# Performance work log

Hardware: AMD Instinct MI355X
Metric: run time of the kernel (lower is better)

## Reference

```python
import jax, jax.numpy as jnp
import numpy as np

BATCH = 2048
IN_DIM = 512          # group input dim
HID = 1024            # meta_output_dim = dim*2
E = 16                # meta_experts_num = num_experts*2
RANK = 2              # lora_rank
EPS = 1e-5


def setup_inputs() -> dict:
    key = jax.random.key(0)
    ks = jax.random.split(key, 8)
    x = jax.random.normal(ks[0], (BATCH, IN_DIM), jnp.float32)
    gate_states = jax.random.normal(ks[1], (BATCH, IN_DIM), jnp.float32)
    expert_indices = jnp.arange(E, dtype=jnp.int64)
    expert_weights = jax.random.normal(ks[2], (E, IN_DIM, HID), jnp.float32) * 0.02
    expert_biases = jnp.zeros((E, HID), jnp.float32)
    bn_weights = jnp.ones((E, HID), jnp.float32)
    bn_biases = jnp.zeros((E, HID), jnp.float32)
    running_mean = jax.random.normal(ks[3], (E, HID), jnp.float32) * 0.1
    running_var = jnp.abs(jax.random.normal(ks[4], (E, HID), jnp.float32)) * 0.5 + 0.5
    gate_weights = jax.random.normal(ks[5], (IN_DIM, E), jnp.float32) * 0.02
    lora_A = jax.random.normal(ks[6], (IN_DIM, RANK), jnp.float32) * 0.02
    lora_B = jax.random.normal(ks[7], (RANK, IN_DIM), jnp.float32) * 0.02
    return dict(x=x, gate_states=gate_states, expert_indices=expert_indices,
                expert_weights=expert_weights, expert_biases=expert_biases,
                bn_weights=bn_weights, bn_biases=bn_biases,
                running_mean=running_mean, running_var=running_var,
                gate_weights=gate_weights, lora_A=lora_A, lora_B=lora_B)


def reference(x, gate_states, expert_indices, expert_weights, expert_biases,
              bn_weights, bn_biases, running_mean, running_var,
              gate_weights, lora_A, lora_B):
    # LoRA feature gate (lora_gate_forward with sigmoid): x * sigmoid(x A B)
    xg = x * jax.nn.sigmoid((x @ lora_A) @ lora_B)          # [B, D]

    # Expert dispatch: gather selected expert params (home_expert_forward)
    W = expert_weights[expert_indices]                        # [E, D, H]
    b = expert_biases[expert_indices]                         # [E, H]
    h = jnp.einsum('bd,edh->ebh', xg, W) + b[:, None, :]      # [E, B, H]

    # Fused inference BatchNorm + SiLU (fused_batch_norm_silu_forward)
    inv = jax.lax.rsqrt(running_var[expert_indices] + EPS)    # [E, H]
    scale = bn_weights[expert_indices] * inv                  # [E, H]
    shift = bn_biases[expert_indices] - running_mean[expert_indices] * scale
    h = h * scale[:, None, :] + shift[:, None, :]
    h = h * jax.nn.sigmoid(h)                                 # SiLU

    # Softmax gate (gate_weights_forward) and weighted combine
    g = jax.nn.softmax(gate_states @ gate_weights, axis=-1)   # [B, E]
    out = jnp.einsum('ebh,be->bh', h, g)                      # [B, H]
    return out
```

## Files before the change

kernel.cpp:

```cpp
#include <hip/hip_runtime.h>
#include <hip/hip_bf16.h>

#define BATCH 2048
#define IN_DIM 512
#define HID 1024
#define NE 16
#define EPSV 1e-5f

typedef __bf16 bf16x8 __attribute__((ext_vector_type(8)));
typedef float floatx4 __attribute__((ext_vector_type(4)));
typedef unsigned short ushort8 __attribute__((ext_vector_type(8)));

__device__ __forceinline__ unsigned short f2bf(float f) {
  unsigned int u = __builtin_bit_cast(unsigned int, f);
  u += 0x7FFFu + ((u >> 16) & 1u);
  return (unsigned short)(u >> 16);
}

__device__ __forceinline__ int get_expert(const int* __restrict__ idx, int e) {
  bool is64 = (idx[1] == 0) && (idx[3] == 0);
  return is64 ? (int)((const long long*)idx)[e] : idx[e];
}

__device__ __forceinline__ void gld16(void* lds, const void* g) {
  __builtin_amdgcn_global_load_lds(
      (const __attribute__((address_space(1))) void*)g,
      (__attribute__((address_space(3))) void*)lds, 16, 0, 0);
}

__global__ __launch_bounds__(256) void prep_all(
    const int* __restrict__ idx, const float* __restrict__ W,
    unsigned short* __restrict__ WT,
    const float* __restrict__ x, const float* __restrict__ gs,
    const float* __restrict__ gw, const float* __restrict__ lA,
    const float* __restrict__ lB,
    unsigned short* __restrict__ xg, float* __restrict__ g,
    const float* __restrict__ bnw, const float* __restrict__ bnb,
    const float* __restrict__ rmean, const float* __restrict__ rvar,
    const float* __restrict__ ebias,
    float* __restrict__ Ac, float* __restrict__ Cc) {
  int bid = blockIdx.x;
  if (bid < 2048) {
    int e = bid >> 7, kt = (bid >> 4) & 7, ht = bid & 15;
    int ie = get_expert(idx, e);
    int k0 = kt * 64, h0 = ht * 64;
    __shared__ float tile[64][65];
    const float* Wp = W + (size_t)ie * IN_DIM * HID;
#pragma unroll
    for (int i = 0; i < 4; ++i) {
      int id = threadIdx.x + i * 256;
      int k = id >> 4, c = (id & 15) * 4;
      float4 v = *(const float4*)(Wp + (size_t)(k0 + k) * HID + h0 + c);
      tile[k][c] = v.x; tile[k][c + 1] = v.y; tile[k][c + 2] = v.z; tile[k][c + 3] = v.w;
    }
    __syncthreads();
#pragma unroll
    for (int i = 0; i < 2; ++i) {
      int id = threadIdx.x + i * 256;
      int h = id >> 3, kc = (id & 7) * 8;
      ushort8 o;
#pragma unroll
      for (int j = 0; j < 8; ++j) o[j] = f2bf(tile[kc + j][h]);
      *(ushort8*)(WT + ((size_t)e * HID + h0 + h) * IN_DIM + k0 + kc) = o;
    }
  } else if (bid < 2560) {
    int lane = threadIdx.x & 63;
    int b = (bid - 2048) * 4 + (threadIdx.x >> 6);
    const float* xrow = x + (size_t)b * IN_DIM;
    const float* grow = gs + (size_t)b * IN_DIM;
    int d0 = lane * 8;
    float4 xa = *(const float4*)(xrow + d0);
    float4 xb = *(const float4*)(xrow + d0 + 4);
    float xv[8] = {xa.x, xa.y, xa.z, xa.w, xb.x, xb.y, xb.z, xb.w};
    float4 ga = *(const float4*)(grow + d0);
    float4 gb = *(const float4*)(grow + d0 + 4);
    float gv[8] = {ga.x, ga.y, ga.z, ga.w, gb.x, gb.y, gb.z, gb.w};

    float u0 = 0.f, u1 = 0.f;
#pragma unroll
    for (int j = 0; j < 8; ++j) {
      float2 a2 = *(const float2*)(lA + (size_t)(d0 + j) * 2);
      u0 += xv[j] * a2.x;
      u1 += xv[j] * a2.y;
    }
#pragma unroll
    for (int off = 1; off < 64; off <<= 1) {
      u0 += __shfl_xor(u0, off);
      u1 += __shfl_xor(u1, off);
    }
    float ge[16];
#pragma unroll
    for (int e = 0; e < 16; ++e) ge[e] = 0.f;
#pragma unroll
    for (int j = 0; j < 8; ++j) {
      float q = gv[j];
      const float4* gwr = (const float4*)(gw + (size_t)(d0 + j) * NE);
      float4 w0 = gwr[0], w1 = gwr[1], w2 = gwr[2], w3 = gwr[3];
      ge[0] += q * w0.x; ge[1] += q * w0.y; ge[2] += q * w0.z; ge[3] += q * w0.w;
      ge[4] += q * w1.x; ge[5] += q * w1.y; ge[6] += q * w1.z; ge[7] += q * w1.w;
      ge[8] += q * w2.x; ge[9] += q * w2.y; ge[10] += q * w2.z; ge[11] += q * w2.w;
      ge[12] += q * w3.x; ge[13] += q * w3.y; ge[14] += q * w3.z; ge[15] += q * w3.w;
    }
#pragma unroll
    for (int off = 1; off < 64; off <<= 1) {
#pragma unroll
      for (int e = 0; e < 16; ++e) ge[e] += __shfl_xor(ge[e], off);
    }
    float m = ge[0];
#pragma unroll
    for (int e = 1; e < 16; ++e) m = fmaxf(m, ge[e]);
    float p[16], s = 0.f;
#pragma unroll
    for (int e = 0; e < 16; ++e) { p[e] = __expf(ge[e] - m); s += p[e]; }
    float inv = 1.f / s;
    if (lane == 0) {
      float* gout = g + (size_t)b * NE;
#pragma unroll
      for (int e = 0; e < 16; ++e) gout[e] = p[e] * inv;
    }
    ushort8 ov;
#pragma unroll
    for (int j = 0; j < 8; ++j) {
      float t = u0 * lB[d0 + j] + u1 * lB[IN_DIM + d0 + j];
      float sg = 1.f / (1.f + __expf(-t));
      ov[j] = f2bf(xv[j] * sg);
    }
    *(ushort8*)(xg + (size_t)b * IN_DIM + d0) = ov;
  } else {
    int t = (bid - 2560) * 256 + threadIdx.x;
    int e = t >> 10, h = t & 1023;
    int ie = get_expert(idx, e);
    size_t o = (size_t)ie * HID + h;
    float scale = bnw[o] * rsqrtf(rvar[o] + EPSV);
    Ac[t] = scale;
    Cc[t] = (ebias[o] - rmean[o]) * scale + bnb[o];
  }
}

__global__ __launch_bounds__(256) void zero_out(float* __restrict__ out) {
  int t = blockIdx.x * 256 + threadIdx.x;
  ((float4*)out)[t] = float4{0.f, 0.f, 0.f, 0.f};
}

__global__ __launch_bounds__(256) void reduce4(const float* __restrict__ sws,
                                               float* __restrict__ out) {
  int t = blockIdx.x * 256 + threadIdx.x;
  const float4* s0 = (const float4*)sws;
  const float4* s1 = s0 + (BATCH * HID / 4);
  const float4* s2 = s1 + (BATCH * HID / 4);
  const float4* s3 = s2 + (BATCH * HID / 4);
  float4 a = s0[t], b = s1[t], c = s2[t], d = s3[t];
  ((float4*)out)[t] = float4{a.x + b.x + c.x + d.x, a.y + b.y + c.y + d.y,
                             a.z + b.z + c.z + d.z, a.w + b.w + c.w + d.w};
}

#define BM 128
#define BN 128
#define KS 32
#define EPB 4

__global__ __launch_bounds__(256, 2) void moe_main(
    const unsigned short* __restrict__ xg, const unsigned short* __restrict__ WT,
    const float* __restrict__ g, const float* __restrict__ Ac,
    const float* __restrict__ Cc, float* __restrict__ splitws,
    float* __restrict__ out, int use_split) {
  __shared__ __align__(16) unsigned short As[2][2][BM * KS];
  __shared__ __align__(16) unsigned short Bs[2][2][BN * KS];
  __shared__ float gS[BM][EPB];

  int tid = threadIdx.x;
  int lane = tid & 63, w = tid >> 6;
  int wr = w >> 1, wc = w & 1;
  int l15 = lane & 15, quad = lane >> 4;

  int bid = blockIdx.x;
  int p = bid >> 7;
  int rowb = (bid >> 3) & 15, colb = bid & 7;
  int row0 = rowb * BM, col0 = colb * BN;
  int e0 = p * EPB;

  for (int i = tid; i < BM * EPB; i += 256) {
    int r = i >> 2, e = i & 3;
    gS[r][e] = g[(size_t)(row0 + r) * NE + e0 + e];
  }

  int dr = lane >> 2, dk = (lane & 3) * 8;
  const unsigned short* gA = xg + (size_t)(row0 + w * 32 + dr) * IN_DIM + dk;
  const unsigned short* gB = WT + ((size_t)e0 * HID + col0 + w * 32 + dr) * IN_DIM + dk;

  auto dma = [&](int t, int buf) {
    int e = t >> 3, s = t & 7;
    size_t aoff = (size_t)s * 64;
    size_t boff = (size_t)e * HID * IN_DIM + s * 64;
#pragma unroll
    for (int kk = 0; kk < 2; ++kk) {
#pragma unroll
      for (int j = 0; j < 2; ++j) {
        gld16(&As[buf][kk][(w * 32 + j * 16) * KS],
              gA + aoff + kk * KS + (size_t)j * 16 * IN_DIM);
        gld16(&Bs[buf][kk][(w * 32 + j * 16) * KS],
              gB + boff + kk * KS + (size_t)j * 16 * IN_DIM);
      }
    }
  };

  floatx4 acc[4][4], oacc[4][4];
#pragma unroll
  for (int rt = 0; rt < 4; ++rt)
#pragma unroll
    for (int ct = 0; ct < 4; ++ct)
#pragma unroll
      for (int r = 0; r < 4; ++r) { acc[rt][ct][r] = 0.f; oacc[rt][ct][r] = 0.f; }

  dma(0, 0);
  __syncthreads();
  int buf = 0;
  for (int t = 0; t < 32; ++t) {
    if (t < 31) dma(t + 1, buf ^ 1);
#pragma unroll
    for (int kk = 0; kk < 2; ++kk) {
      bf16x8 af[4], bfv[4];
#pragma unroll
      for (int rt = 0; rt < 4; ++rt)
        af[rt] = *(const bf16x8*)&As[buf][kk][(wr * 64 + rt * 16 + l15) * KS + quad * 8];
#pragma unroll
      for (int ct = 0; ct < 4; ++ct)
        bfv[ct] = *(const bf16x8*)&Bs[buf][kk][(wc * 64 + ct * 16 + l15) * KS + quad * 8];
#pragma unroll
      for (int rt = 0; rt < 4; ++rt)
#pragma unroll
        for (int ct = 0; ct < 4; ++ct)
          acc[rt][ct] = __builtin_amdgcn_mfma_f32_16x16x32_bf16(af[rt], bfv[ct], acc[rt][ct], 0, 0, 0);
    }
    if ((t & 7) == 7) {
      int e = t >> 3;
#pragma unroll
      for (int ct = 0; ct < 4; ++ct) {
        int colg = col0 + wc * 64 + ct * 16 + l15;
        float A_ = Ac[(e0 + e) * HID + colg];
        float C_ = Cc[(e0 + e) * HID + colg];
#pragma unroll
        for (int rt = 0; rt < 4; ++rt) {
          int rb = wr * 64 + rt * 16 + quad * 4;
#pragma unroll
          for (int r = 0; r < 4; ++r) {
            float gvw = gS[rb + r][e];
            float z = A_ * acc[rt][ct][r] + C_;
            float sg = 1.f / (1.f + __expf(-z));
            oacc[rt][ct][r] += gvw * z * sg;
            acc[rt][ct][r] = 0.f;
          }
        }
      }
    }
    __syncthreads();
    buf ^= 1;
  }

  if (use_split) {
    float* sout = splitws + (size_t)p * BATCH * HID;
#pragma unroll
    for (int rt = 0; rt < 4; ++rt)
#pragma unroll
      for (int ct = 0; ct < 4; ++ct)
#pragma unroll
        for (int r = 0; r < 4; ++r)
          sout[(size_t)(row0 + wr * 64 + rt * 16 + quad * 4 + r) * HID +
               col0 + wc * 64 + ct * 16 + l15] = oacc[rt][ct][r];
  } else {
#pragma unroll
    for (int rt = 0; rt < 4; ++rt)
#pragma unroll
      for (int ct = 0; ct < 4; ++ct)
#pragma unroll
        for (int r = 0; r < 4; ++r)
          atomicAdd(&out[(size_t)(row0 + wr * 64 + rt * 16 + quad * 4 + r) * HID +
                         col0 + wc * 64 + ct * 16 + l15], oacc[rt][ct][r]);
  }
}

extern "C" void kernel_launch(void* const* d_in, const int* in_sizes, int n_in,
                              void* d_out, int out_size, void* d_ws, size_t ws_size,
                              hipStream_t stream) {
  const float* x     = (const float*)d_in[0];
  const float* gs    = (const float*)d_in[1];
  const int*   idx   = (const int*)d_in[2];
  const float* W     = (const float*)d_in[3];
  const float* ebias = (const float*)d_in[4];
  const float* bnw   = (const float*)d_in[5];
  const float* bnb   = (const float*)d_in[6];
  const float* rmean = (const float*)d_in[7];
  const float* rvar  = (const float*)d_in[8];
  const float* gw    = (const float*)d_in[9];
  const float* lA    = (const float*)d_in[10];
  const float* lB    = (const float*)d_in[11];
  float* out = (float*)d_out;

  char* ws = (char*)d_ws;
  unsigned short* WT = (unsigned short*)ws;
  unsigned short* xg = (unsigned short*)(ws + 16777216);
  float* g    = (float*)(ws + 18874368);
  float* Acf  = (float*)(ws + 19005440);
  float* Ccf  = (float*)(ws + 19070976);
  float* sws  = (float*)(ws + 19136512);
  int use_split = (ws_size >= 19136512 + 4ull * BATCH * HID * 4) ? 1 : 0;

  prep_all<<<dim3(2624), dim3(256), 0, stream>>>(
      idx, W, WT, x, gs, gw, lA, lB, xg, g, bnw, bnb, rmean, rvar, ebias, Acf, Ccf);
  if (!use_split)
    zero_out<<<dim3(BATCH * HID / 1024), dim3(256), 0, stream>>>(out);
  moe_main<<<dim3((BATCH / BM) * (HID / BN) * (NE / EPB)), dim3(256), 0, stream>>>(
      xg, WT, g, Acf, Ccf, sws, out, use_split);
  if (use_split)
    reduce4<<<dim3(BATCH * HID / 1024), dim3(256), 0, stream>>>(sws, out);
}
```

Measured before the change: 179.1 us.

## Use 512-thread blocks and load A fragments directly from global memory

The main MoE GEMM kernel moves to 512 threads with 8 waves in a 4x2 grid, so each wave owns a 32x64 sub-tile. The xg activation tile is no longer staged through LDS; each wave reads its bf16x8 A fragments straight from global memory every K step. Only the expert weight tile stays double-buffered in LDS. This cuts LDS traffic and per-thread register use to raise occupancy, but A is now fetched redundantly per wave and without prefetch, so global or L2 latency may be exposed.

```diff
diff --git a/kernel.cpp b/kernel.cpp
--- a/kernel.cpp
+++ b/kernel.cpp
@@ -159,12 +159,11 @@
 #define KS 32
 #define EPB 4
 
-__global__ __launch_bounds__(256, 2) void moe_main(
+__global__ __launch_bounds__(512, 4) void moe_main(
     const unsigned short* __restrict__ xg, const unsigned short* __restrict__ WT,
     const float* __restrict__ g, const float* __restrict__ Ac,
     const float* __restrict__ Cc, float* __restrict__ splitws,
     float* __restrict__ out, int use_split) {
-  __shared__ __align__(16) unsigned short As[2][2][BM * KS];
   __shared__ __align__(16) unsigned short Bs[2][2][BN * KS];
   __shared__ float gS[BM][EPB];
 
@@ -179,34 +178,27 @@
   int row0 = rowb * BM, col0 = colb * BN;
   int e0 = p * EPB;
 
-  for (int i = tid; i < BM * EPB; i += 256) {
-    int r = i >> 2, e = i & 3;
+  {
+    int r = tid >> 2, e = tid & 3;
     gS[r][e] = g[(size_t)(row0 + r) * NE + e0 + e];
   }
 
   int dr = lane >> 2, dk = (lane & 3) * 8;
-  const unsigned short* gA = xg + (size_t)(row0 + w * 32 + dr) * IN_DIM + dk;
-  const unsigned short* gB = WT + ((size_t)e0 * HID + col0 + w * 32 + dr) * IN_DIM + dk;
-
+  const unsigned short* gB =
+      WT + ((size_t)e0 * HID + col0 + w * 16 + dr) * IN_DIM + dk;
   auto dma = [&](int t, int buf) {
-    int e = t >> 3, s = t & 7;
-    size_t aoff = (size_t)s * 64;
-    size_t boff = (size_t)e * HID * IN_DIM + s * 64;
-#pragma unroll
-    for (int kk = 0; kk < 2; ++kk) {
-#pragma unroll
-      for (int j = 0; j < 2; ++j) {
-        gld16(&As[buf][kk][(w * 32 + j * 16) * KS],
-              gA + aoff + kk * KS + (size_t)j * 16 * IN_DIM);
-        gld16(&Bs[buf][kk][(w * 32 + j * 16) * KS],
-              gB + boff + kk * KS + (size_t)j * 16 * IN_DIM);
-      }
-    }
+    size_t off = (size_t)(t >> 3) * HID * IN_DIM + (size_t)(t & 7) * 64;
+#pragma unroll
+    for (int kk = 0; kk < 2; ++kk)
+      gld16(&Bs[buf][kk][(w * 16) * KS], gB + off + kk * KS);
   };
 
-  floatx4 acc[4][4], oacc[4][4];
-#pragma unroll
-  for (int rt = 0; rt < 4; ++rt)
+  const unsigned short* gA =
+      xg + (size_t)(row0 + wr * 32 + l15) * IN_DIM + quad * 8;
+
+  floatx4 acc[2][4], oacc[2][4];
+#pragma unroll
+  for (int rt = 0; rt < 2; ++rt)
 #pragma unroll
     for (int ct = 0; ct < 4; ++ct)
 #pragma unroll
@@ -216,21 +208,25 @@
   __syncthreads();
   int buf = 0;
   for (int t = 0; t < 32; ++t) {
+    int k0 = (t & 7) * 64;
+    bf16x8 a[2][2];
+#pragma unroll
+    for (int rt = 0; rt < 2; ++rt)
+#pragma unroll
+      for (int kk = 0; kk < 2; ++kk)
+        a[rt][kk] = *(const bf16x8*)(gA + (size_t)rt * 16 * IN_DIM + k0 + kk * 32);
     if (t < 31) dma(t + 1, buf ^ 1);
 #pragma unroll
     for (int kk = 0; kk < 2; ++kk) {
-      bf16x8 af[4], bfv[4];
-#pragma unroll
-      for (int rt = 0; rt < 4; ++rt)
-        af[rt] = *(const bf16x8*)&As[buf][kk][(wr * 64 + rt * 16 + l15) * KS + quad * 8];
+      bf16x8 bfv[4];
 #pragma unroll
       for (int ct = 0; ct < 4; ++ct)
         bfv[ct] = *(const bf16x8*)&Bs[buf][kk][(wc * 64 + ct * 16 + l15) * KS + quad * 8];
 #pragma unroll
-      for (int rt = 0; rt < 4; ++rt)
+      for (int rt = 0; rt < 2; ++rt)
 #pragma unroll
         for (int ct = 0; ct < 4; ++ct)
-          acc[rt][ct] = __builtin_amdgcn_mfma_f32_16x16x32_bf16(af[rt], bfv[ct], acc[rt][ct], 0, 0, 0);
+          acc[rt][ct] = __builtin_amdgcn_mfma_f32_16x16x32_bf16(a[rt][kk], bfv[ct], acc[rt][ct], 0, 0, 0);
     }
     if ((t & 7) == 7) {
       int e = t >> 3;
@@ -240,8 +236,8 @@
         float A_ = Ac[(e0 + e) * HID + colg];
         float C_ = Cc[(e0 + e) * HID + colg];
 #pragma unroll
-        for (int rt = 0; rt < 4; ++rt) {
-          int rb = wr * 64 + rt * 16 + quad * 4;
+        for (int rt = 0; rt < 2; ++rt) {
+          int rb = wr * 32 + rt * 16 + quad * 4;
 #pragma unroll
           for (int r = 0; r < 4; ++r) {
             float gvw = gS[rb + r][e];
@@ -260,21 +256,21 @@
   if (use_split) {
     float* sout = splitws + (size_t)p * BATCH * HID;
 #pragma unroll
-    for (int rt = 0; rt < 4; ++rt)
+    for (int rt = 0; rt < 2; ++rt)
 #pragma unroll
       for (int ct = 0; ct < 4; ++ct)
 #pragma unroll
         for (int r = 0; r < 4; ++r)
-          sout[(size_t)(row0 + wr * 64 + rt * 16 + quad * 4 + r) * HID +
+          sout[(size_t)(row0 + wr * 32 + rt * 16 + quad * 4 + r) * HID +
                col0 + wc * 64 + ct * 16 + l15] = oacc[rt][ct][r];
   } else {
 #pragma unroll
-    for (int rt = 0; rt < 4; ++rt)
+    for (int rt = 0; rt < 2; ++rt)
 #pragma unroll
       for (int ct = 0; ct < 4; ++ct)
 #pragma unroll
         for (int r = 0; r < 4; ++r)
-          atomicAdd(&out[(size_t)(row0 + wr * 64 + rt * 16 + quad * 4 + r) * HID +
+          atomicAdd(&out[(size_t)(row0 + wr * 32 + rt * 16 + quad * 4 + r) * HID +
                          col0 + wc * 64 + ct * 16 + l15], oacc[rt][ct][r]);
   }
 }
@@ -309,7 +305,7 @@
       idx, W, WT, x, gs, gw, lA, lB, xg, g, bnw, bnb, rmean, rvar, ebias, Acf, Ccf);
   if (!use_split)
     zero_out<<<dim3(BATCH * HID / 1024), dim3(256), 0, stream>>>(out);
-  moe_main<<<dim3((BATCH / BM) * (HID / BN) * (NE / EPB)), dim3(256), 0, stream>>>(
+  moe_main<<<dim3((BATCH / BM) * (HID / BN) * (NE / EPB)), dim3(512), 0, stream>>>(
       xg, WT, g, Acf, Ccf, sws, out, use_split);
   if (use_split)
     reduce4<<<dim3(BATCH * HID / 1024), dim3(256), 0, stream>>>(sws, out);
```

After: 201.1 us. 1.12x slower.
